# Kernel optimization log

Measured on AMD Instinct MI355X. Metric: run time of the kernel, lower is better.

Reference implementation:

```python
import jax, jax.numpy as jnp
import numpy as np

EPS = 1e-5

def layer_norm(x, w, b):
    mu = jnp.mean(x, axis=-1, keepdims=True)
    var = jnp.mean(jnp.square(x - mu), axis=-1, keepdims=True)
    return (x - mu) * jax.lax.rsqrt(var + EPS) * w + b

def setup_inputs() -> dict:
    key = jax.random.key(0)
    ks = jax.random.split(key, 8)
    B, T, C = 8, 512, 768
    s = 1.0 / np.sqrt(C)
    s4 = 1.0 / np.sqrt(4 * C)
    return {
        "x": jax.random.normal(ks[0], (B, T, C), dtype=jnp.float32),
        "ln1_w": jnp.ones((C,), jnp.float32),
        "ln1_b": jnp.zeros((C,), jnp.float32),
        "Wr": jax.random.normal(ks[1], (C, C), dtype=jnp.float32) * s,
        "Wk": jax.random.normal(ks[2], (C, C), dtype=jnp.float32) * s,
        "Wv": jax.random.normal(ks[3], (C, C), dtype=jnp.float32) * s,
        "time_mix_w": jnp.ones((C,), jnp.float32),  # torch init: torch.ones(n_embd)
        "Wrouter": jax.random.normal(ks[4], (C, C), dtype=jnp.float32) * s,
        "ln2_w": jnp.ones((C,), jnp.float32),
        "ln2_b": jnp.zeros((C,), jnp.float32),
        "Wck": jax.random.normal(ks[5], (4 * C, C), dtype=jnp.float32) * s,
        "Wcv": jax.random.normal(ks[6], (C, 4 * C), dtype=jnp.float32) * s4,
    }

def reference(x, ln1_w, ln1_b, Wr, Wk, Wv, time_mix_w, Wrouter, ln2_w, ln2_b, Wck, Wcv):
    B, T, C = x.shape
    xx = layer_norm(x, ln1_w, ln1_b)
    r = xx @ Wr.T
    k = xx @ Wk.T
    v = xx @ Wv.T
    w = -jnp.exp(time_mix_w)                        # (C,) negative per-channel decay rate
    idx = jnp.arange(T)
    diff = jnp.clip(idx[:, None] - idx[None, :], 0).astype(x.dtype)  # (T,T) t-j clamped at 0
    causal = jnp.tril(jnp.ones((T, T), x.dtype))
    decay = jnp.exp(w[:, None, None] * diff[None]) * causal          # (C,T,T)
    kv = k * v                                                       # (B,T,C)
    # wkv[b,t,c] = sum_j decay[c,t,j] * kv[b,j,c]
    wkv = jnp.einsum('ctj,bjc->btc', decay, kv)
    routed_wkv = wkv * jax.nn.sigmoid(xx @ Wrouter.T)
    x = x + r * routed_wkv
    xx2 = layer_norm(x, ln2_w, ln2_b)
    k_cm = jnp.square(jax.nn.relu(xx2 @ Wck.T))                      # (B,T,4C)
    return x + k_cm @ Wcv.T
```

## Files before the change

### kernel.cpp

```cpp
#include <hip/hip_runtime.h>
#include <hip/hip_bf16.h>

typedef __bf16 bf16_t;
typedef __bf16 bf16x8 __attribute__((ext_vector_type(8)));
typedef __bf16 bf16x4 __attribute__((ext_vector_type(4)));
typedef float  f32x4  __attribute__((ext_vector_type(4)));

#define LN_EPS 1e-5f


typedef __attribute__((address_space(1))) void gvoid_t;
typedef __attribute__((address_space(3))) void lvoid_t;
__device__ __forceinline__ void glds16(const void* g, void* l) {
    __builtin_amdgcn_global_load_lds((gvoid_t*)g, (lvoid_t*)l, 16, 0, 0);
}

__global__ __launch_bounds__(256) void k_cvt4(const float* __restrict__ s0,
                                              const float* __restrict__ s1,
                                              const float* __restrict__ s2,
                                              const float* __restrict__ s3,
                                              bf16_t* __restrict__ dst, int n4) {
    const float* s = (blockIdx.y == 0) ? s0 : (blockIdx.y == 1) ? s1 : (blockIdx.y == 2) ? s2 : s3;
    bf16_t* d = dst + (size_t)blockIdx.y * ((size_t)n4 * 4);
    int i = blockIdx.x * 256 + threadIdx.x;
    if (i < n4) {
        float4 v = ((const float4*)s)[i];
        bf16x4 o;
        o.x = (bf16_t)v.x; o.y = (bf16_t)v.y; o.z = (bf16_t)v.z; o.w = (bf16_t)v.w;
        ((bf16x4*)d)[i] = o;
    }
}

__global__ __launch_bounds__(256) void k_cvt2(const float* __restrict__ s0,
                                              const float* __restrict__ s1,
                                              bf16_t* __restrict__ dst, int n4) {
    const float* s = (blockIdx.y == 0) ? s0 : s1;
    bf16_t* d = dst + (size_t)blockIdx.y * ((size_t)n4 * 4);
    int i = blockIdx.x * 256 + threadIdx.x;
    if (i < n4) {
        float4 v = ((const float4*)s)[i];
        bf16x4 o;
        o.x = (bf16_t)v.x; o.y = (bf16_t)v.y; o.z = (bf16_t)v.z; o.w = (bf16_t)v.w;
        ((bf16x4*)d)[i] = o;
    }
}

__global__ __launch_bounds__(256) void k_ln(const float* __restrict__ x,
                                            const float* __restrict__ w,
                                            const float* __restrict__ b,
                                            bf16_t* __restrict__ out, int C) {
    int row = blockIdx.x;
    const float* xr = x + (long)row * C;
    int tid = threadIdx.x;
    float s = 0.f, s2 = 0.f;
    for (int i = tid; i < C; i += 256) { float v = xr[i]; s += v; s2 += v * v; }
    for (int m = 32; m; m >>= 1) { s += __shfl_xor(s, m, 64); s2 += __shfl_xor(s2, m, 64); }
    __shared__ float red[8];
    int wv = tid >> 6;
    if ((tid & 63) == 0) { red[wv] = s; red[4 + wv] = s2; }
    __syncthreads();
    float ts  = red[0] + red[1] + red[2] + red[3];
    float ts2 = red[4] + red[5] + red[6] + red[7];
    float mu  = ts / C;
    float var = ts2 / C - mu * mu;
    float rstd = rsqrtf(var + LN_EPS);
    bf16_t* orow = out + (long)row * C;
    for (int i = tid; i < C; i += 256)
        orow[i] = (bf16_t)((xr[i] - mu) * rstd * w[i] + b[i]);
}

template <int EPI>
__global__ __launch_bounds__(256) void k_gemm_bt(const bf16_t* __restrict__ A,
                                                 const bf16_t* __restrict__ Bw,
                                                 void* __restrict__ Cout,
                                                 const float* __restrict__ aux,
                                                 int N, int K, int nbn) {
    __shared__ __align__(16) bf16_t As[128][32];
    __shared__ __align__(16) bf16_t Bs[128][32];
    const int tid  = threadIdx.x;
    const int lane = tid & 63, wid = tid >> 6;
    const int wm = (wid >> 1) * 64, wn = (wid & 1) * 64;

    int nwg = gridDim.x;
    int cpx = nwg >> 3;
    int bid = blockIdx.x;
    int swz = (bid & 7) * cpx + (bid >> 3);
    int bm = swz / nbn, bn = swz % nbn;

    const int fr = lane & 15, ko = (lane >> 4) * 8;

    f32x4 acc[4][4];
#pragma unroll
    for (int i = 0; i < 4; i++)
#pragma unroll
        for (int j = 0; j < 4; j++) acc[i][j] = (f32x4){0.f, 0.f, 0.f, 0.f};

    const int srow = wid * 32 + (lane >> 2);
    const int scol = (lane & 3) * 8;
    const bf16_t* Ag = A  + (size_t)(bm * 128 + srow) * K + scol;
    const bf16_t* Bg = Bw + (size_t)(bn * 128 + srow) * K + scol;
    const size_t rowK16 = (size_t)16 * K;
    bf16_t* lA0 = &As[wid * 32][0];
    bf16_t* lA1 = &As[wid * 32 + 16][0];
    bf16_t* lB0 = &Bs[wid * 32][0];
    bf16_t* lB1 = &Bs[wid * 32 + 16][0];

    for (int kt = 0; kt < K; kt += 32) {
        glds16(Ag + kt,          lA0);
        glds16(Ag + kt + rowK16, lA1);
        glds16(Bg + kt,          lB0);
        glds16(Bg + kt + rowK16, lB1);
        __syncthreads();
        bf16x8 af[4], bfr[4];
#pragma unroll
        for (int mi = 0; mi < 4; mi++) af[mi]  = *(const bf16x8*)&As[wm + mi * 16 + fr][ko];
#pragma unroll
        for (int ni = 0; ni < 4; ni++) bfr[ni] = *(const bf16x8*)&Bs[wn + ni * 16 + fr][ko];
#pragma unroll
        for (int mi = 0; mi < 4; mi++)
#pragma unroll
            for (int ni = 0; ni < 4; ni++)
                acc[mi][ni] = __builtin_amdgcn_mfma_f32_16x16x32_bf16(af[mi], bfr[ni], acc[mi][ni], 0, 0, 0);
        __syncthreads();
    }

    const int row0 = bm * 128 + wm, col0 = bn * 128 + wn;
#pragma unroll
    for (int mi = 0; mi < 4; mi++) {
#pragma unroll
        for (int ni = 0; ni < 4; ni++) {
            int row = row0 + mi * 16 + (lane >> 4) * 4;
            int col = col0 + ni * 16 + (lane & 15);
#pragma unroll
            for (int r = 0; r < 4; r++) {
                float val = acc[mi][ni][r];
                size_t off = (size_t)(row + r) * N + col;
                if (EPI == 0) {
                    ((bf16_t*)Cout)[off] = (bf16_t)val;
                } else if (EPI == 1) {
                    float t = fmaxf(val, 0.f);
                    ((bf16_t*)Cout)[off] = (bf16_t)(t * t);
                } else {
                    ((float*)Cout)[off] = aux[off] + val;
                }
            }
        }
    }
}

__global__ __launch_bounds__(256) void k_scan_local(const bf16_t* __restrict__ y4,
                                                    const float* __restrict__ tmw,
                                                    float* __restrict__ wkvl,
                                                    float* __restrict__ states) {
    int idx = blockIdx.x * 256 + threadIdx.x;
    int c   = idx % 768;
    int rem = idx / 768;
    int ch  = rem & 15;
    int b   = rem >> 4;
    float d = expf(-expf(tmw[c]));
    const bf16_t* base = y4 + ((size_t)(b * 512 + ch * 32)) * 3072 + c;
    float*        wout = wkvl + ((size_t)(b * 512 + ch * 32)) * 768 + c;
    float s = 0.f;
#pragma unroll 4
    for (int i = 0; i < 32; i++) {
        float kk = (float)base[(size_t)i * 3072 + 768];
        float vv = (float)base[(size_t)i * 3072 + 1536];
        s = s * d + kk * vv;
        wout[(size_t)i * 768] = s;
    }
    states[idx] = s;
}

__global__ __launch_bounds__(256) void k_scan_carry(const float* __restrict__ states,
                                                    const float* __restrict__ tmw,
                                                    float* __restrict__ carries) {
    int idx = blockIdx.x * 256 + threadIdx.x;
    int c = idx % 768, b = idx / 768;
    float dL = expf(-expf(tmw[c]) * 32.f);
    float s = 0.f;
    for (int ch = 0; ch < 16; ch++) {
        size_t o = ((size_t)(b * 16 + ch)) * 768 + c;
        carries[o] = s;
        s = s * dL + states[o];
    }
}

__global__ __launch_bounds__(256) void k_mix_ln(const bf16_t* __restrict__ y4,
                                                const float* __restrict__ wkvl,
                                                const float* __restrict__ carries,
                                                const float* __restrict__ tmw,
                                                const float* __restrict__ x,
                                                const float* __restrict__ w2,
                                                const float* __restrict__ b2,
                                                float* __restrict__ x1,
                                                bf16_t* __restrict__ xx2) {
    int bt = blockIdx.x;
    int t = bt & 511, b = bt >> 9;
    int tid = threadIdx.x;
    const bf16_t* yrow = y4 + (size_t)bt * 3072;
    const float*  wl   = wkvl + (size_t)bt * 768;
    const float*  cr   = carries + ((size_t)(b * 16) + (t >> 5)) * 768;
    const float*  xr   = x + (size_t)bt * 768;
    float tn = (float)((t & 31) + 1);

    float vals[3];
    float s = 0.f, s2 = 0.f;
#pragma unroll
    for (int j = 0; j < 3; j++) {
        int c = tid + j * 256;
        float rr = (float)yrow[c];
        float gg = (float)yrow[c + 2304];
        float wk = wl[c] + cr[c] * expf(-expf(tmw[c]) * tn);
        float sig = 1.f / (1.f + expf(-gg));
        float o = fmaf(rr, wk * sig, xr[c]);
        vals[j] = o; s += o; s2 += o * o;
    }
    for (int m = 32; m; m >>= 1) { s += __shfl_xor(s, m, 64); s2 += __shfl_xor(s2, m, 64); }
    __shared__ float red[8];
    int wv = tid >> 6;
    if ((tid & 63) == 0) { red[wv] = s; red[4 + wv] = s2; }
    __syncthreads();
    float ts  = red[0] + red[1] + red[2] + red[3];
    float ts2 = red[4] + red[5] + red[6] + red[7];
    float mu  = ts * (1.f / 768.f);
    float var = ts2 * (1.f / 768.f) - mu * mu;
    float rstd = rsqrtf(var + LN_EPS);
    float* x1r = x1 + (size_t)bt * 768;
    bf16_t* xo = xx2 + (size_t)bt * 768;
#pragma unroll
    for (int j = 0; j < 3; j++) {
        int c = tid + j * 256;
        x1r[c] = vals[j];
        xo[c] = (bf16_t)((vals[j] - mu) * rstd * w2[c] + b2[c]);
    }
}

extern "C" void kernel_launch(void* const* d_in, const int* in_sizes, int n_in,
                              void* d_out, int out_size, void* d_ws, size_t ws_size,
                              hipStream_t stream) {
    const float* x    = (const float*)d_in[0];
    const float* ln1w = (const float*)d_in[1];
    const float* ln1b = (const float*)d_in[2];
    const float* Wr   = (const float*)d_in[3];
    const float* Wk   = (const float*)d_in[4];
    const float* Wv   = (const float*)d_in[5];
    const float* tmw  = (const float*)d_in[6];
    const float* Wrt  = (const float*)d_in[7];
    const float* ln2w = (const float*)d_in[8];
    const float* ln2b = (const float*)d_in[9];
    const float* Wck  = (const float*)d_in[10];
    const float* Wcv  = (const float*)d_in[11];
    float* out = (float*)d_out;
    char* ws = (char*)d_ws;

    bf16_t* xx     = (bf16_t*)(ws + 0);
    bf16_t* wcat   = (bf16_t*)(ws + 6291456);
    bf16_t* wckb   = (bf16_t*)(ws + 11010048);
    bf16_t* wcvb   = (bf16_t*)(ws + 15728640);
    bf16_t* y4     = (bf16_t*)(ws + 20447232);
    bf16_t* kcm    = (bf16_t*)(ws + 20447232);
    float*  wkvl   = (float*)(ws + 70778880);
    float*  states = (float*)(ws + 83361792);
    float*  carr   = (float*)(ws + 83755008);
    float*  x1     = (float*)(ws + 84148224);

    const int n768 = 768 * 768 / 4;
    const int nbig = 3072 * 768 / 4;
    k_cvt4<<<dim3(576, 4), dim3(256), 0, stream>>>(Wr, Wk, Wv, Wrt, wcat, n768);
    k_cvt2<<<dim3(2304, 2), dim3(256), 0, stream>>>(Wck, Wcv, wckb, nbig);

    k_ln<<<dim3(4096), dim3(256), 0, stream>>>(x, ln1w, ln1b, xx, 768);

    k_gemm_bt<0><<<dim3(768), dim3(256), 0, stream>>>(xx, wcat, (void*)y4, nullptr, 3072, 768, 24);

    k_scan_local<<<dim3(384), dim3(256), 0, stream>>>(y4, tmw, wkvl, states);
    k_scan_carry<<<dim3(24), dim3(256), 0, stream>>>(states, tmw, carr);
    k_mix_ln<<<dim3(4096), dim3(256), 0, stream>>>(y4, wkvl, carr, tmw, x, ln2w, ln2b, x1, xx);

    k_gemm_bt<1><<<dim3(768), dim3(256), 0, stream>>>(xx, wckb, (void*)kcm, nullptr, 3072, 768, 24);

    k_gemm_bt<2><<<dim3(192), dim3(256), 0, stream>>>(kcm, wcvb, (void*)out, x1, 768, 3072, 6);
}
```

Before: 175.7 us.

## Double-buffer GEMM LDS tiles and use narrower N tile for final projection

Adds a second LDS buffer to the bf16 MFMA GEMM so the next K-slice is loaded via global_load_lds while the current slice is computed, leaving one barrier per iteration instead of two. The kernel is templated on the N tile width, and the final 3072-to-768 projection switches to a 64-wide N tile so it launches 384 workgroups instead of 192, filling more compute units. In exchange the kernel uses twice the LDS, and the narrower tile gives less reuse per block on the last GEMM.

```diff
diff --git a/kernel.cpp b/kernel.cpp
--- a/kernel.cpp
+++ b/kernel.cpp
@@ -69,17 +69,22 @@
         orow[i] = (bf16_t)((xr[i] - mu) * rstd * w[i] + b[i]);
 }
 
-template <int EPI>
+template <int EPI, int BN>
 __global__ __launch_bounds__(256) void k_gemm_bt(const bf16_t* __restrict__ A,
                                                  const bf16_t* __restrict__ Bw,
                                                  void* __restrict__ Cout,
                                                  const float* __restrict__ aux,
                                                  int N, int K, int nbn) {
-    __shared__ __align__(16) bf16_t As[128][32];
-    __shared__ __align__(16) bf16_t Bs[128][32];
+    constexpr int NI = BN / 32;
+    constexpr int WN = BN / 2;
+    constexpr int ABUF = 128 * 32;
+    constexpr int BBUF = BN * 32;
+    __shared__ __align__(16) bf16_t As[2][128][32];
+    __shared__ __align__(16) bf16_t Bs[2][BN][32];
+
     const int tid  = threadIdx.x;
     const int lane = tid & 63, wid = tid >> 6;
-    const int wm = (wid >> 1) * 64, wn = (wid & 1) * 64;
+    const int wm = (wid >> 1) * 64, wn = (wid & 1) * WN;
 
     int nwg = gridDim.x;
     int cpx = nwg >> 3;
@@ -89,46 +94,61 @@
 
     const int fr = lane & 15, ko = (lane >> 4) * 8;
 
-    f32x4 acc[4][4];
+    f32x4 acc[4][NI];
 #pragma unroll
     for (int i = 0; i < 4; i++)
 #pragma unroll
-        for (int j = 0; j < 4; j++) acc[i][j] = (f32x4){0.f, 0.f, 0.f, 0.f};
-
-    const int srow = wid * 32 + (lane >> 2);
+        for (int j = 0; j < NI; j++) acc[i][j] = (f32x4){0.f, 0.f, 0.f, 0.f};
+
+    const int srow = wid * 16 + (lane >> 2);
     const int scol = (lane & 3) * 8;
     const bf16_t* Ag = A  + (size_t)(bm * 128 + srow) * K + scol;
-    const bf16_t* Bg = Bw + (size_t)(bn * 128 + srow) * K + scol;
-    const size_t rowK16 = (size_t)16 * K;
-    bf16_t* lA0 = &As[wid * 32][0];
-    bf16_t* lA1 = &As[wid * 32 + 16][0];
-    bf16_t* lB0 = &Bs[wid * 32][0];
-    bf16_t* lB1 = &Bs[wid * 32 + 16][0];
-
-    for (int kt = 0; kt < K; kt += 32) {
-        glds16(Ag + kt,          lA0);
-        glds16(Ag + kt + rowK16, lA1);
-        glds16(Bg + kt,          lB0);
-        glds16(Bg + kt + rowK16, lB1);
+    const bf16_t* Bg = Bw + (size_t)(bn * BN + srow) * K + scol;
+    const size_t rowK64 = (size_t)64 * K;
+    bf16_t* lA = &As[0][wid * 16][0];
+    bf16_t* lB = &Bs[0][wid * 16][0];
+
+#define STAGE(buf, kt)                                                          \
+    do {                                                                        \
+        glds16(Ag + (kt),          lA + (buf) * ABUF);                          \
+        glds16(Ag + (kt) + rowK64, lA + (buf) * ABUF + 64 * 32);                \
+        glds16(Bg + (kt),          lB + (buf) * BBUF);                          \
+        if (BN == 128) glds16(Bg + (kt) + rowK64, lB + (buf) * BBUF + 64 * 32); \
+    } while (0)
+
+#define COMPUTE(buf)                                                                         \
+    do {                                                                                     \
+        bf16x8 af[4], bfr[NI];                                                               \
+        _Pragma("unroll")                                                                    \
+        for (int mi = 0; mi < 4; mi++) af[mi] = *(const bf16x8*)&As[buf][wm + mi * 16 + fr][ko]; \
+        _Pragma("unroll")                                                                    \
+        for (int ni = 0; ni < NI; ni++) bfr[ni] = *(const bf16x8*)&Bs[buf][wn + ni * 16 + fr][ko]; \
+        _Pragma("unroll")                                                                    \
+        for (int mi = 0; mi < 4; mi++)                                                       \
+            _Pragma("unroll")                                                                \
+            for (int ni = 0; ni < NI; ni++)                                                  \
+                acc[mi][ni] = __builtin_amdgcn_mfma_f32_16x16x32_bf16(af[mi], bfr[ni], acc[mi][ni], 0, 0, 0); \
+    } while (0)
+
+    STAGE(0, 0);
+    __syncthreads();
+    int cur = 0;
+    for (int kt = 0; kt < K - 32; kt += 32) {
+        STAGE(cur ^ 1, kt + 32);
+        COMPUTE(cur);
         __syncthreads();
-        bf16x8 af[4], bfr[4];
-#pragma unroll
-        for (int mi = 0; mi < 4; mi++) af[mi]  = *(const bf16x8*)&As[wm + mi * 16 + fr][ko];
-#pragma unroll
-        for (int ni = 0; ni < 4; ni++) bfr[ni] = *(const bf16x8*)&Bs[wn + ni * 16 + fr][ko];
-#pragma unroll
-        for (int mi = 0; mi < 4; mi++)
-#pragma unroll
-            for (int ni = 0; ni < 4; ni++)
-                acc[mi][ni] = __builtin_amdgcn_mfma_f32_16x16x32_bf16(af[mi], bfr[ni], acc[mi][ni], 0, 0, 0);
-        __syncthreads();
-    }
-
-    const int row0 = bm * 128 + wm, col0 = bn * 128 + wn;
+        cur ^= 1;
+    }
+    COMPUTE(cur);
+
+#undef STAGE
+#undef COMPUTE
+
+    const int row0 = bm * 128 + wm, col0 = bn * BN + wn;
 #pragma unroll
     for (int mi = 0; mi < 4; mi++) {
 #pragma unroll
-        for (int ni = 0; ni < 4; ni++) {
+        for (int ni = 0; ni < NI; ni++) {
             int row = row0 + mi * 16 + (lane >> 4) * 4;
             int col = col0 + ni * 16 + (lane & 15);
 #pragma unroll
@@ -271,13 +291,13 @@
 
     k_ln<<<dim3(4096), dim3(256), 0, stream>>>(x, ln1w, ln1b, xx, 768);
 
-    k_gemm_bt<0><<<dim3(768), dim3(256), 0, stream>>>(xx, wcat, (void*)y4, nullptr, 3072, 768, 24);
+    k_gemm_bt<0, 128><<<dim3(768), dim3(256), 0, stream>>>(xx, wcat, (void*)y4, nullptr, 3072, 768, 24);
 
     k_scan_local<<<dim3(384), dim3(256), 0, stream>>>(y4, tmw, wkvl, states);
     k_scan_carry<<<dim3(24), dim3(256), 0, stream>>>(states, tmw, carr);
     k_mix_ln<<<dim3(4096), dim3(256), 0, stream>>>(y4, wkvl, carr, tmw, x, ln2w, ln2b, x1, xx);
 
-    k_gemm_bt<1><<<dim3(768), dim3(256), 0, stream>>>(xx, wckb, (void*)kcm, nullptr, 3072, 768, 24);
-
-    k_gemm_bt<2><<<dim3(192), dim3(256), 0, stream>>>(kcm, wcvb, (void*)out, x1, 768, 3072, 6);
-}
+    k_gemm_bt<1, 128><<<dim3(768), dim3(256), 0, stream>>>(xx, wckb, (void*)kcm, nullptr, 3072, 768, 24);
+
+    k_gemm_bt<2, 64><<<dim3(384), dim3(256), 0, stream>>>(kcm, wcvb, (void*)out, x1, 768, 3072, 12);
+}
```

Result: faster. 158.4 us (-9.8%).
